# Kernel tuning notes

Measured on AMD Instinct MI355X. Metric: run time of the kernel, lower is better.

The kernel has to match this reference:

```python
import jax, jax.numpy as jnp
import numpy as np

DIM = 2048
N_HEADS = 16
HEAD_DIM = DIM // N_HEADS
ROPE_BASE = 10000.0


def _rope_cos_sin(seq_len, head_dim, dtype):
    inv_freq = 1.0 / (ROPE_BASE ** (jnp.arange(0, head_dim, 2, dtype=jnp.float32) / head_dim))
    t = jnp.arange(seq_len, dtype=jnp.float32)
    freqs = jnp.einsum('s,d->sd', t, inv_freq)          # (S, hd/2)
    emb = jnp.concatenate([freqs, freqs], axis=-1)       # (S, hd)
    return jnp.cos(emb).astype(dtype), jnp.sin(emb).astype(dtype)


def _rotate_half(x):
    x1, x2 = jnp.split(x, 2, axis=-1)
    return jnp.concatenate([-x2, x1], axis=-1)


def _apply_rope(x, cos, sin):
    # x: (B, H, S, hd); cos/sin: (S, hd)
    return x * cos[None, None] + _rotate_half(x) * sin[None, None]


def setup_inputs() -> dict:
    key = jax.random.key(0)
    ks = jax.random.split(key, 5)
    B, S = 2, 2048
    scale = 1.0 / np.sqrt(DIM)
    return {
        'x': jax.random.normal(ks[0], (B, S, DIM), dtype=jnp.float32),
        'Wq': jax.random.normal(ks[1], (DIM, DIM), dtype=jnp.float32) * scale,
        'Wk': jax.random.normal(ks[2], (DIM, DIM), dtype=jnp.float32) * scale,
        'Wv': jax.random.normal(ks[3], (DIM, DIM), dtype=jnp.float32) * scale,
        'Wo': jax.random.normal(ks[4], (DIM, DIM), dtype=jnp.float32) * scale,
    }


def reference(x, Wq, Wk, Wv, Wo):
    B, S, _ = x.shape
    scale = HEAD_DIM ** -0.5

    def proj(W):
        # torch Linear: x @ W.T ; reshape to (B, H, S, hd)
        return (x @ W.T).reshape(B, S, N_HEADS, HEAD_DIM).transpose(0, 2, 1, 3)

    q, k, v = proj(Wq), proj(Wk), proj(Wv)
    cos, sin = _rope_cos_sin(S, HEAD_DIM, x.dtype)
    q = _apply_rope(q, cos, sin)
    k = _apply_rope(k, cos, sin)

    scores = jnp.einsum('bhqd,bhkd->bhqk', q, k) * scale  # (B,H,S,S)
    causal = jnp.triu(jnp.ones((S, S), dtype=bool), k=1)
    scores = jnp.where(causal[None, None], -jnp.inf, scores)
    attn = jax.nn.softmax(scores.astype(jnp.float32), axis=-1).astype(q.dtype)
    out = jnp.einsum('bhqk,bhkd->bhqd', attn, v)          # (B,H,S,hd)
    out = out.transpose(0, 2, 1, 3).reshape(B, S, DIM)
    return out @ Wo.T
```

## Files before the change

kernel.cpp:

```cpp
#include <hip/hip_runtime.h>


#define SEQ 2048
#define DMODEL 2048
#define NH 16
#define HD 128

typedef __attribute__((ext_vector_type(8))) short bf16x8;
typedef __attribute__((ext_vector_type(4))) float f32x4;

__device__ __forceinline__ unsigned short f2bf(float f) {
  unsigned int u = __float_as_uint(f);
  u += 0x7fffu + ((u >> 16) & 1u);
  return (unsigned short)(u >> 16);
}

__device__ __forceinline__ void g2l16(const void* g, void* l) {
  __builtin_amdgcn_global_load_lds((const __attribute__((address_space(1))) void*)g,
                                   (__attribute__((address_space(3))) void*)l,
                                   16, 0, 0);
}

__device__ __forceinline__ f32x4 mfma16(bf16x8 a, bf16x8 b, f32x4 c) {
  return __builtin_amdgcn_mfma_f32_16x16x32_bf16(a, b, c, 0, 0, 0);
}

template <int CTRL>
__device__ __forceinline__ float dpp_ror(float v) {
  return __int_as_float(__builtin_amdgcn_mov_dpp(__float_as_int(v), CTRL, 0xf, 0xf, false));
}
__device__ __forceinline__ float red_max16(float v) {
  v = fmaxf(v, dpp_ror<0x128>(v));
  v = fmaxf(v, dpp_ror<0x124>(v));
  v = fmaxf(v, dpp_ror<0x122>(v));
  v = fmaxf(v, dpp_ror<0x121>(v));
  return v;
}
__device__ __forceinline__ float red_sum16(float v) {
  v += dpp_ror<0x128>(v);
  v += dpp_ror<0x124>(v);
  v += dpp_ror<0x122>(v);
  v += dpp_ror<0x121>(v);
  return v;
}

__global__ __launch_bounds__(256) void cvt_all(const float* __restrict__ x,
                                               const float* __restrict__ wq,
                                               const float* __restrict__ wk,
                                               const float* __restrict__ wv,
                                               const float* __restrict__ wo,
                                               unsigned short* __restrict__ dst0,
                                               float2* __restrict__ rtab) {
  const int b = blockIdx.x;
  if (b >= 24576) {
    const int idx = (b - 24576) * 256 + threadIdx.x;
    const int s = idx >> 6, d = idx & 63;
    float sn, cs;
    sincosf((float)s * exp2f(-0.20762050593046f * (float)d), &sn, &cs);
    rtab[idx] = make_float2(cs, sn);
    return;
  }
  const float* src;
  unsigned short* dst;
  int idx, r = -1;
  if (b < 8192) {
    src = x; dst = dst0; idx = b * 256 + threadIdx.x;
  } else {
    r = (b - 8192) >> 12;
    src = (r == 0) ? wq : (r == 1) ? wk : (r == 2) ? wv : wo;
    dst = dst0 + (size_t)2 * SEQ * DMODEL + (size_t)r * DMODEL * DMODEL;
    idx = ((b - 8192) & 4095) * 256 + threadIdx.x;
  }
  const float4 v = ((const float4*)src)[idx];
  ushort4 o;
  o.x = f2bf(v.x); o.y = f2bf(v.y); o.z = f2bf(v.z); o.w = f2bf(v.w);
  int widx = idx;
  if (r == 0 || r == 1) {
    const int row = idx >> 9, col = idx & 511;
    const int o_ = row & 127;
    const int e = (((o_ >> 4) & 3) << 5) | (((o_ >> 6) & 1) << 4) | (o_ & 15);
    widx = (((row & ~127) | e) << 9) | col;
  }
  ((ushort4*)dst)[widx] = o;
}

template <int MODE>
__global__ __launch_bounds__(512, 2) void gemm_pipe(
    const unsigned short* __restrict__ A,
    const unsigned short* __restrict__ B,
    unsigned short* __restrict__ obf,
    float* __restrict__ of32,
    const float2* __restrict__ rtab) {
  __shared__ unsigned short lds[3 * 24576];
  const int nb = blockIdx.x, mb = blockIdx.y;
  const int M0 = mb * 256;
  const int t = threadIdx.x;
  const int w = t >> 6, lane = t & 63, l15 = lane & 15, quad = lane >> 4;
  const int g = lane >> 3, j = lane & 7;
  const int wm = w >> 1, wn = w & 1;

  const unsigned short* Abase = A + (size_t)M0 * DMODEL;
  const unsigned short* Bbase = B + (size_t)nb * 128 * DMODEL;

  f32x4 acc[4][4] = {};

  auto stage = [&](int buf, int k0, int i0) {
#pragma unroll
    for (int i = 0; i < 3; ++i) {
      const int u = w * 6 + i0 + i;
      if (u < 32) {
        const int row = u * 8 + g;
        g2l16(Abase + (size_t)row * DMODEL + k0 + ((j ^ g) << 3),
              &lds[buf * 24576 + u * 512]);
      } else {
        const int row = (u - 32) * 8 + g;
        g2l16(Bbase + (size_t)row * DMODEL + k0 + ((j ^ g) << 3),
              &lds[buf * 24576 + 16384 + (u - 32) * 512]);
      }
    }
  };

  auto comp = [&](int buf, int kc) {
    const int c = kc * 4 + quad;
    const unsigned short* As_ = &lds[buf * 24576];
    const unsigned short* Bs_ = &lds[buf * 24576 + 16384];
    bf16x8 af[4], bf[4];
#pragma unroll
    for (int mt = 0; mt < 4; ++mt) {
      const int m = wm * 64 + mt * 16 + l15;
      af[mt] = *(const bf16x8*)&As_[m * 64 + ((c ^ (m & 7)) << 3)];
    }
#pragma unroll
    for (int nt = 0; nt < 4; ++nt) {
      const int n = wn * 64 + nt * 16 + l15;
      bf[nt] = *(const bf16x8*)&Bs_[n * 64 + ((c ^ (n & 7)) << 3)];
    }
#pragma unroll
    for (int nt = 0; nt < 4; ++nt)
#pragma unroll
      for (int mt = 0; mt < 4; ++mt)
        acc[mt][nt] = mfma16(af[mt], bf[nt], acc[mt][nt]);
  };

  stage(0, 0, 0);
  stage(0, 0, 3);
  stage(1, 64, 0);
  stage(1, 64, 3);
  asm volatile("s_waitcnt vmcnt(6)\n\ts_barrier" ::: "memory");

  int buf = 0, b2 = 2;
  for (int tt = 0; tt < 32; ++tt) {
    const int k0 = tt * 64;
    if (tt < 30) stage(b2, k0 + 128, 0);
    comp(buf, 0);
    if (tt < 30) stage(b2, k0 + 128, 3);
    comp(buf, 1);
    if (tt < 30) {
      asm volatile("s_waitcnt vmcnt(6)\n\ts_barrier" ::: "memory");
    } else if (tt == 30) {
      asm volatile("s_waitcnt vmcnt(0)\n\ts_barrier" ::: "memory");
    }
    buf = (buf == 2) ? 0 : buf + 1;
    b2 = (b2 == 2) ? 0 : b2 + 1;
  }

  if (MODE == 0) {
    const size_t NX = (size_t)2 * SEQ * DMODEL;
    const int z = nb >> 4;
    const int h = nb & 15;
    if (z < 2) {
      const float qscale = (z == 0) ? 0.1275174356f : 1.0f;
      unsigned short* O = obf + (size_t)z * NX;
#pragma unroll
      for (int mt = 0; mt < 4; ++mt)
#pragma unroll
        for (int reg = 0; reg < 4; ++reg) {
          const int m = M0 + wm * 64 + mt * 16 + quad * 4 + reg;
          const int bb = m >> 11, s = m & 2047;
          unsigned short* ob = O + ((size_t)(bb * NH + h) * SEQ + s) * HD;
#pragma unroll
          for (int p = 0; p < 2; ++p) {
            const int q = wn * 2 + p;
            const float2 cs = rtab[s * 64 + q * 16 + l15];
            const float x1 = acc[mt][2 * p][reg], x2 = acc[mt][2 * p + 1][reg];
            ob[wn * 64 + (2 * p) * 16 + l15] = f2bf((x1 * cs.x - x2 * cs.y) * qscale);
            ob[wn * 64 + (2 * p + 1) * 16 + l15] = f2bf((x2 * cs.x + x1 * cs.y) * qscale);
          }
        }
    } else {
      unsigned short* Vb = obf + 2 * NX + (size_t)h * HD * SEQ;
#pragma unroll
      for (int mt = 0; mt < 4; ++mt)
#pragma unroll
        for (int reg = 0; reg < 4; ++reg) {
          const int m = M0 + wm * 64 + mt * 16 + quad * 4 + reg;
          const int bb = m >> 11, s = m & 2047;
          unsigned short* ob = Vb + (size_t)bb * NH * HD * SEQ;
#pragma unroll
          for (int nt = 0; nt < 4; ++nt)
            ob[(size_t)(wn * 64 + nt * 16 + l15) * SEQ + s] = f2bf(acc[mt][nt][reg]);
        }
    }
  } else {
#pragma unroll
    for (int mt = 0; mt < 4; ++mt)
#pragma unroll
      for (int reg = 0; reg < 4; ++reg) {
        const int m = M0 + wm * 64 + mt * 16 + quad * 4 + reg;
#pragma unroll
        for (int nt = 0; nt < 4; ++nt)
          of32[(size_t)m * DMODEL + nb * 128 + wn * 64 + nt * 16 + l15] =
              acc[mt][nt][reg];
      }
  }
}

__global__ __launch_bounds__(256) void attn_kernel(const unsigned short* __restrict__ Q,
                                                   const unsigned short* __restrict__ K,
                                                   const unsigned short* __restrict__ Vt,
                                                   unsigned short* __restrict__ Oa) {
  __shared__ unsigned short Ks[256 * 64];
  __shared__ unsigned short Vs[256 * 64];
  const int gid = blockIdx.x;
  const int bh = gid & 31;
  const int pr = gid >> 5;
  const unsigned short* Qb = Q + (size_t)bh * SEQ * HD;
  const unsigned short* Kb = K + (size_t)bh * SEQ * HD;
  const unsigned short* Vb = Vt + (size_t)bh * HD * SEQ;
  const int t = threadIdx.x;
  const int w = t >> 6, lane = t & 63, l15 = lane & 15, quad = lane >> 4;
  const int g = lane >> 3, j = lane & 7;
  const int b = bh >> 4, h = bh & 15;

  for (int half = 0; half < 2; ++half) {
    const int qt = half ? 15 - pr : pr;

    bf16x8 qf[2][4];
#pragma unroll
    for (int mt = 0; mt < 2; ++mt)
#pragma unroll
      for (int ch = 0; ch < 4; ++ch)
        qf[mt][ch] = *(const bf16x8*)(Qb + (size_t)(qt * 128 + w * 32 + mt * 16 + l15) * HD +
                                      ch * 32 + quad * 8);

    f32x4 o[2][8] = {};
    float mrow[2][4], lrow[2][4];
#pragma unroll
    for (int mt = 0; mt < 2; ++mt)
#pragma unroll
      for (int reg = 0; reg < 4; ++reg) { mrow[mt][reg] = -1e30f; lrow[mt][reg] = 0.f; }

    for (int kt = 0; kt <= qt; ++kt) {
      __syncthreads();
#pragma unroll
      for (int r = 0; r < 16; ++r) {
        const int u = r * 4 + w;
        if (u < 32) {
          const int vrow = u * 8 + g, key = vrow >> 1;
          const int ck = j ^ (key & 7);
          g2l16(Kb + (size_t)(kt * 128 + key) * HD + (vrow & 1) * 64 + ck * 8, &Ks[u * 512]);
        } else {
          const int u2 = u - 32;
          const int vrow = u2 * 8 + g, d = vrow >> 1;
          const int cv = j ^ (d & 7);
          g2l16(Vb + (size_t)d * SEQ + kt * 128 + (vrow & 1) * 64 + cv * 8, &Vs[u2 * 512]);
        }
      }
      __syncthreads();

      f32x4 s[2][8] = {};
#pragma unroll
      for (int ch = 0; ch < 4; ++ch) {
        const int hh = ch >> 1, c = (ch & 1) * 4 + quad;
#pragma unroll
        for (int nt = 0; nt < 8; ++nt) {
          const int n = nt * 16 + l15;
          const bf16x8 bv = *(const bf16x8*)&Ks[(n * 2 + hh) * 64 + ((c ^ (n & 7)) << 3)];
#pragma unroll
          for (int mt = 0; mt < 2; ++mt) s[mt][nt] = mfma16(qf[mt][ch], bv, s[mt][nt]);
        }
      }

      if (kt == qt) {
#pragma unroll
        for (int mt = 0; mt < 2; ++mt)
#pragma unroll
          for (int nt = 0; nt < 8; ++nt)
#pragma unroll
            for (int reg = 0; reg < 4; ++reg) {
              const int rr = w * 32 + mt * 16 + quad * 4 + reg;
              const int cc = nt * 16 + l15;
              if (cc > rr) s[mt][nt][reg] = -1e30f;
            }
      }

#pragma unroll
      for (int mt = 0; mt < 2; ++mt)
#pragma unroll
        for (int reg = 0; reg < 4; ++reg) {
          float vmax = s[mt][0][reg];
#pragma unroll
          for (int nt = 1; nt < 8; ++nt) vmax = fmaxf(vmax, s[mt][nt][reg]);
          vmax = red_max16(vmax);
          const float mo = mrow[mt][reg];
          const float mn = fmaxf(mo, vmax);
          const float alpha = exp2f(mo - mn);
          mrow[mt][reg] = mn;
          float rs = 0.f;
#pragma unroll
          for (int nt = 0; nt < 8; ++nt) {
            const float p_ = exp2f(s[mt][nt][reg] - mn);
            s[mt][nt][reg] = p_;
            rs += p_;
          }
          rs = red_sum16(rs);
          lrow[mt][reg] = lrow[mt][reg] * alpha + rs;
#pragma unroll
          for (int nt = 0; nt < 8; ++nt) o[mt][nt][reg] *= alpha;
        }

      __syncthreads();

      unsigned short* Pw = &Ks[w * 4096];
#pragma unroll
      for (int mt = 0; mt < 2; ++mt)
#pragma unroll
        for (int nt = 0; nt < 8; ++nt)
#pragma unroll
          for (int reg = 0; reg < 4; ++reg) {
            const int rr = mt * 16 + quad * 4 + reg;
            const int key = nt * 16 + l15;
            Pw[(key >> 3) * 256 + rr * 8 + (key & 7)] = f2bf(s[mt][nt][reg]);
          }

#pragma unroll
      for (int ch = 0; ch < 4; ++ch) {
        const int kh = ch >> 1, c = (ch & 1) * 4 + quad;
        bf16x8 pa[2];
#pragma unroll
        for (int mt = 0; mt < 2; ++mt)
          pa[mt] = *(const bf16x8*)&Pw[(ch * 4 + quad) * 256 + (mt * 16 + l15) * 8];
#pragma unroll
        for (int nt = 0; nt < 8; ++nt) {
          const int d = nt * 16 + l15;
          const bf16x8 vv = *(const bf16x8*)&Vs[(d * 2 + kh) * 64 + ((c ^ (d & 7)) << 3)];
#pragma unroll
          for (int mt = 0; mt < 2; ++mt) o[mt][nt] = mfma16(pa[mt], vv, o[mt][nt]);
        }
      }
    }

#pragma unroll
    for (int mt = 0; mt < 2; ++mt)
#pragma unroll
      for (int reg = 0; reg < 4; ++reg) {
        const int sq = qt * 128 + w * 32 + mt * 16 + quad * 4 + reg;
        const float inv_l = 1.0f / lrow[mt][reg];
        unsigned short* ob = Oa + (size_t)(b * SEQ + sq) * DMODEL + h * HD;
#pragma unroll
        for (int nt = 0; nt < 8; ++nt) ob[nt * 16 + l15] = f2bf(o[mt][nt][reg] * inv_l);
      }
  }
}

extern "C" void kernel_launch(void* const* d_in, const int* in_sizes, int n_in,
                              void* d_out, int out_size, void* d_ws, size_t ws_size,
                              hipStream_t stream) {
  const float* x = (const float*)d_in[0];
  const float* Wq = (const float*)d_in[1];
  const float* Wk = (const float*)d_in[2];
  const float* Wv = (const float*)d_in[3];
  const float* Wo = (const float*)d_in[4];
  float* out = (float*)d_out;

  const size_t NX = (size_t)2 * SEQ * DMODEL;
  const size_t NW = (size_t)DMODEL * DMODEL;
  unsigned short* ws = (unsigned short*)d_ws;
  unsigned short* xb = ws;
  unsigned short* wqb = xb + NX;
  unsigned short* wkb = wqb + NW;
  unsigned short* wvb = wkb + NW;
  unsigned short* wob = wvb + NW;
  unsigned short* qb = wob + NW;
  unsigned short* kb = qb + NX;
  unsigned short* vb = kb + NX;
  unsigned short* ab = vb + NX;
  float2* rtab = (float2*)(ab + NX);

  cvt_all<<<25088, 256, 0, stream>>>(x, Wq, Wk, Wv, Wo, ws, rtab);
  gemm_pipe<0><<<dim3(48, 16), 512, 0, stream>>>(xb, wqb, qb, nullptr, rtab);
  attn_kernel<<<256, 256, 0, stream>>>(qb, kb, vb, ab);
  gemm_pipe<1><<<dim3(16, 16), 512, 0, stream>>>(ab, wob, nullptr, out, nullptr);
}
```

Before: 371.5 us.

## Halve attention query tile to 64 rows and double grid, add lazy rescale

```diff
diff --git a/kernel.cpp b/kernel.cpp
--- a/kernel.cpp
+++ b/kernel.cpp
@@ -231,26 +231,24 @@
   const int w = t >> 6, lane = t & 63, l15 = lane & 15, quad = lane >> 4;
   const int g = lane >> 3, j = lane & 7;
   const int b = bh >> 4, h = bh & 15;
+  const int r2r = l15 ^ ((l15 >> 2) & 2);
 
   for (int half = 0; half < 2; ++half) {
-    const int qt = half ? 15 - pr : pr;
-
-    bf16x8 qf[2][4];
-#pragma unroll
-    for (int mt = 0; mt < 2; ++mt)
-#pragma unroll
-      for (int ch = 0; ch < 4; ++ch)
-        qf[mt][ch] = *(const bf16x8*)(Qb + (size_t)(qt * 128 + w * 32 + mt * 16 + l15) * HD +
-                                      ch * 32 + quad * 8);
-
-    f32x4 o[2][8] = {};
-    float mrow[2][4], lrow[2][4];
-#pragma unroll
-    for (int mt = 0; mt < 2; ++mt)
-#pragma unroll
-      for (int reg = 0; reg < 4; ++reg) { mrow[mt][reg] = -1e30f; lrow[mt][reg] = 0.f; }
-
-    for (int kt = 0; kt <= qt; ++kt) {
+    const int qt = half ? 31 - pr : pr;
+    const int ktmax = (qt * 64 + 63) >> 7;
+
+    bf16x8 qf[4];
+#pragma unroll
+    for (int ch = 0; ch < 4; ++ch)
+      qf[ch] = *(const bf16x8*)(Qb + (size_t)(qt * 64 + w * 16 + l15) * HD +
+                                ch * 32 + quad * 8);
+
+    f32x4 o[8] = {};
+    float mrow[4], lrow[4];
+#pragma unroll
+    for (int reg = 0; reg < 4; ++reg) { mrow[reg] = -1e30f; lrow[reg] = 0.f; }
+
+    for (int kt = 0; kt <= ktmax; ++kt) {
       __syncthreads();
 #pragma unroll
       for (int r = 0; r < 16; ++r) {
@@ -268,98 +266,106 @@
       }
       __syncthreads();
 
-      f32x4 s[2][8] = {};
+      const bool halftile = (kt == ktmax) && !(qt & 1);
+      f32x4 s[8] = {};
+      __builtin_amdgcn_s_setprio(1);
 #pragma unroll
       for (int ch = 0; ch < 4; ++ch) {
         const int hh = ch >> 1, c = (ch & 1) * 4 + quad;
 #pragma unroll
-        for (int nt = 0; nt < 8; ++nt) {
+        for (int nt = 0; nt < 4; ++nt) {
           const int n = nt * 16 + l15;
           const bf16x8 bv = *(const bf16x8*)&Ks[(n * 2 + hh) * 64 + ((c ^ (n & 7)) << 3)];
-#pragma unroll
-          for (int mt = 0; mt < 2; ++mt) s[mt][nt] = mfma16(qf[mt][ch], bv, s[mt][nt]);
-        }
-      }
-
-      if (kt == qt) {
-#pragma unroll
-        for (int mt = 0; mt < 2; ++mt)
-#pragma unroll
-          for (int nt = 0; nt < 8; ++nt)
-#pragma unroll
-            for (int reg = 0; reg < 4; ++reg) {
-              const int rr = w * 32 + mt * 16 + quad * 4 + reg;
-              const int cc = nt * 16 + l15;
-              if (cc > rr) s[mt][nt][reg] = -1e30f;
-            }
-      }
-
-#pragma unroll
-      for (int mt = 0; mt < 2; ++mt)
+          s[nt] = mfma16(qf[ch], bv, s[nt]);
+        }
+      }
+      if (!halftile) {
+#pragma unroll
+        for (int ch = 0; ch < 4; ++ch) {
+          const int hh = ch >> 1, c = (ch & 1) * 4 + quad;
+#pragma unroll
+          for (int nt = 4; nt < 8; ++nt) {
+            const int n = nt * 16 + l15;
+            const bf16x8 bv = *(const bf16x8*)&Ks[(n * 2 + hh) * 64 + ((c ^ (n & 7)) << 3)];
+            s[nt] = mfma16(qf[ch], bv, s[nt]);
+          }
+        }
+      }
+      __builtin_amdgcn_s_setprio(0);
+
+      if (kt == ktmax) {
+#pragma unroll
+        for (int nt = 0; nt < 8; ++nt)
+#pragma unroll
+          for (int reg = 0; reg < 4; ++reg) {
+            const int rr = qt * 64 + w * 16 + quad * 4 + reg;
+            const int cc = kt * 128 + nt * 16 + l15;
+            if (cc > rr) s[nt][reg] = -1e30f;
+          }
+      }
+
+#pragma unroll
+      for (int reg = 0; reg < 4; ++reg) {
+        float vmax = s[0][reg];
+#pragma unroll
+        for (int nt = 1; nt < 8; ++nt) vmax = fmaxf(vmax, s[nt][reg]);
+        vmax = red_max16(vmax);
+        const float mo = mrow[reg];
+        float mn = mo;
+        if (!__all(vmax <= mo + 8.0f)) {
+          mn = fmaxf(mo, vmax);
+          const float alpha = exp2f(mo - mn);
+          mrow[reg] = mn;
+          lrow[reg] *= alpha;
+#pragma unroll
+          for (int nt = 0; nt < 8; ++nt) o[nt][reg] *= alpha;
+        }
+        float rs = 0.f;
+#pragma unroll
+        for (int nt = 0; nt < 8; ++nt) {
+          const float p_ = exp2f(s[nt][reg] - mn);
+          s[nt][reg] = p_;
+          rs += p_;
+        }
+        rs = red_sum16(rs);
+        lrow[reg] += rs;
+      }
+
+      __syncthreads();
+
+      unsigned short* Pw = &Ks[w * 2048];
+#pragma unroll
+      for (int nt = 0; nt < 8; ++nt)
 #pragma unroll
         for (int reg = 0; reg < 4; ++reg) {
-          float vmax = s[mt][0][reg];
-#pragma unroll
-          for (int nt = 1; nt < 8; ++nt) vmax = fmaxf(vmax, s[mt][nt][reg]);
-          vmax = red_max16(vmax);
-          const float mo = mrow[mt][reg];
-          const float mn = fmaxf(mo, vmax);
-          const float alpha = exp2f(mo - mn);
-          mrow[mt][reg] = mn;
-          float rs = 0.f;
-#pragma unroll
-          for (int nt = 0; nt < 8; ++nt) {
-            const float p_ = exp2f(s[mt][nt][reg] - mn);
-            s[mt][nt][reg] = p_;
-            rs += p_;
-          }
-          rs = red_sum16(rs);
-          lrow[mt][reg] = lrow[mt][reg] * alpha + rs;
-#pragma unroll
-          for (int nt = 0; nt < 8; ++nt) o[mt][nt][reg] *= alpha;
-        }
-
-      __syncthreads();
-
-      unsigned short* Pw = &Ks[w * 4096];
-#pragma unroll
-      for (int mt = 0; mt < 2; ++mt)
-#pragma unroll
-        for (int nt = 0; nt < 8; ++nt)
-#pragma unroll
-          for (int reg = 0; reg < 4; ++reg) {
-            const int rr = mt * 16 + quad * 4 + reg;
-            const int key = nt * 16 + l15;
-            Pw[(key >> 3) * 256 + rr * 8 + (key & 7)] = f2bf(s[mt][nt][reg]);
-          }
-
+          const int r2 = quad * 4 + (reg ^ (quad & 2));
+          const int key = nt * 16 + l15;
+          Pw[(key >> 3) * 128 + r2 * 8 + (key & 7)] = f2bf(s[nt][reg]);
+        }
+
+      __builtin_amdgcn_s_setprio(1);
 #pragma unroll
       for (int ch = 0; ch < 4; ++ch) {
         const int kh = ch >> 1, c = (ch & 1) * 4 + quad;
-        bf16x8 pa[2];
-#pragma unroll
-        for (int mt = 0; mt < 2; ++mt)
-          pa[mt] = *(const bf16x8*)&Pw[(ch * 4 + quad) * 256 + (mt * 16 + l15) * 8];
+        const bf16x8 pa = *(const bf16x8*)&Pw[(ch * 4 + quad) * 128 + r2r * 8];
 #pragma unroll
         for (int nt = 0; nt < 8; ++nt) {
           const int d = nt * 16 + l15;
           const bf16x8 vv = *(const bf16x8*)&Vs[(d * 2 + kh) * 64 + ((c ^ (d & 7)) << 3)];
-#pragma unroll
-          for (int mt = 0; mt < 2; ++mt) o[mt][nt] = mfma16(pa[mt], vv, o[mt][nt]);
-        }
-      }
-    }
-
-#pragma unroll
-    for (int mt = 0; mt < 2; ++mt)
-#pragma unroll
-      for (int reg = 0; reg < 4; ++reg) {
-        const int sq = qt * 128 + w * 32 + mt * 16 + quad * 4 + reg;
-        const float inv_l = 1.0f / lrow[mt][reg];
-        unsigned short* ob = Oa + (size_t)(b * SEQ + sq) * DMODEL + h * HD;
-#pragma unroll
-        for (int nt = 0; nt < 8; ++nt) ob[nt * 16 + l15] = f2bf(o[mt][nt][reg] * inv_l);
-      }
+          o[nt] = mfma16(pa, vv, o[nt]);
+        }
+      }
+      __builtin_amdgcn_s_setprio(0);
+    }
+
+#pragma unroll
+    for (int reg = 0; reg < 4; ++reg) {
+      const int sq = qt * 64 + w * 16 + quad * 4 + reg;
+      const float inv_l = 1.0f / lrow[reg];
+      unsigned short* ob = Oa + (size_t)(b * SEQ + sq) * DMODEL + h * HD;
+#pragma unroll
+      for (int nt = 0; nt < 8; ++nt) ob[nt * 16 + l15] = f2bf(o[nt][reg] * inv_l);
+    }
   }
 }
 
@@ -389,6 +395,6 @@
 
   cvt_all<<<25088, 256, 0, stream>>>(x, Wq, Wk, Wv, Wo, ws, rtab);
   gemm_pipe<0><<<dim3(48, 16), 512, 0, stream>>>(xb, wqb, qb, nullptr, rtab);
-  attn_kernel<<<256, 256, 0, stream>>>(qb, kb, vb, ab);
+  attn_kernel<<<512, 256, 0, stream>>>(qb, kb, vb, ab);
   gemm_pipe<1><<<dim3(16, 16), 512, 0, stream>>>(ab, wob, nullptr, out, nullptr);
 }
```

After: 412.7 us. +11.1%, slower.
